# Kernel optimization log

Hardware: AMD Instinct MI355X
Metric: run time of the kernel (lower is better)

Reference implementation:

```python
import jax, jax.numpy as jnp
import numpy as np

N_NODES, N_FEAT, EIG, HID = 20000, 128, 32, 64
N_EDGES = 640000
TEMP = 1.0
NUM_DROP = int(N_NODES * N_FEAT * 0.1)  # num_drop_ratio = 0.1
EPS_LOG = 1e-8


def setup_inputs() -> dict:
    key = jax.random.key(0)
    ks = jax.random.split(key, 9)
    x = jax.random.normal(ks[0], (N_NODES, N_FEAT), dtype=jnp.float32)
    edge_index = jax.random.randint(ks[1], (2, N_EDGES), 0, N_NODES, dtype=jnp.int64)
    edge_weights = jax.random.uniform(ks[2], (N_EDGES,), dtype=jnp.float32)
    x_eigen_distance = jax.random.normal(ks[3], (N_NODES, N_FEAT, EIG), dtype=jnp.float32)
    uni_rand = jax.random.uniform(ks[4], (N_NODES * N_FEAT, 2), dtype=jnp.float32,
                                  minval=1e-6, maxval=1.0 - 1e-6)
    # prob_encoder params: Linear(EIG->HID), ReLU, Linear(HID->2)
    W1 = jax.random.normal(ks[5], (EIG, HID), dtype=jnp.float32) / np.sqrt(EIG)
    b1 = jnp.zeros((HID,), dtype=jnp.float32)
    W2 = jax.random.normal(ks[6], (HID, 2), dtype=jnp.float32) / np.sqrt(HID)
    b2 = jnp.zeros((2,), dtype=jnp.float32)
    return {"x": x, "edge_index": edge_index, "edge_weights": edge_weights,
            "x_eigen_distance": x_eigen_distance, "uni_rand": uni_rand,
            "W1": W1, "b1": b1, "W2": W2, "b2": b2}


def reference(x, edge_index, edge_weights, x_eigen_distance, uni_rand, W1, b1, W2, b2):
    # flatten to [N_NODES*N_FEAT, EIG]
    flat = x_eigen_distance.reshape(-1, x_eigen_distance.shape[-1])
    h = jax.nn.relu(flat @ W1 + b1)          # [M, HID]
    logits = h @ W2 + b2                     # [M, 2]
    logits = jnp.log(jax.nn.softmax(logits, axis=1) + EPS_LOG)
    gumbel = -jnp.log(-jnp.log(uni_rand))    # gumbel noise from uniform
    y = jax.nn.softmax((logits + gumbel) / TEMP, axis=1)
    poss = jnp.clip(1.0 - y[:, 0], 1e-6, 1.0)  # [M]
    neg_vals, idx = jax.lax.top_k(-poss, NUM_DROP)  # smallest NUM_DROP
    vals = -neg_vals
    x_new = x.reshape(-1).at[idx].multiply(vals).reshape(x.shape)
    return x_new, edge_index, edge_weights
```

## Files before the change

kernel.cpp:

```cpp
#include <hip/hip_runtime.h>
#include <hip/hip_bf16.h>

#define N_NODES 20000
#define N_FEAT  128
#define EIG     32
#define HID     64
#define N_EDGES 640000
#define M_ROWS  (N_NODES * N_FEAT)
#define K_DROP  256000
#define NBINS   16384
#define LIST_CAP 4096
#define NTILES  (M_ROWS / 16)
#define NBLK    2560

#define POSS_BYTES ((size_t)M_ROWS * 4)
#define HIST_BYTES (NBINS * 4)
#define META_WORDS 16

typedef __attribute__((ext_vector_type(8))) short short8;
typedef __attribute__((ext_vector_type(4))) float floatx4;

__device__ __forceinline__ short f2bf(float f) {
  unsigned u = __float_as_uint(f);
  unsigned r = u + 0x7fffu + ((u >> 16) & 1u);
  return (short)(r >> 16);
}

__device__ __forceinline__ short2 f2bf2(float x, float y) {
  float2 f; f.x = x; f.y = y;
  __hip_bfloat162 h = __float22bfloat162_rn(f);
  union { __hip_bfloat162 h2; short2 s2; } u;
  u.h2 = h;
  return u.s2;
}

__device__ __forceinline__ int bin_of(float ps) {
  int b = (int)(ps * (float)NBINS);
  if (b > NBINS - 1) b = NBINS - 1;
  if (b < 0) b = 0;
  return b;
}

__global__ __launch_bounds__(256) void poss_kernel(
    const float* __restrict__ eig, const float* __restrict__ uni,
    const float* __restrict__ W1, const float* __restrict__ b1,
    const float* __restrict__ W2, const float* __restrict__ b2,
    float* __restrict__ poss, unsigned* __restrict__ hist)
{
  const int wave = threadIdx.x >> 6;
  const int lane = threadIdx.x & 63;
  const int col  = lane & 15;
  const int quad = lane >> 4;
  const int STR  = NBLK * 4;

  short8 bfrag[4];
  #pragma unroll
  for (int t = 0; t < 4; ++t)
    #pragma unroll
    for (int j = 0; j < 8; ++j)
      bfrag[t][j] = f2bf(W1[(quad * 8 + j) * HID + 16 * t + col]);

  float b1v[4], wd[4];
  #pragma unroll
  for (int t = 0; t < 4; ++t) {
    int n = 16 * t + col;
    b1v[t] = b1[n];
    wd[t] = W2[2 * n + 1] - W2[2 * n + 0];
  }
  const float bd = b2[1] - b2[0];

  const bool epi = (col < 4);
  const int  epirow = quad * 4 + col;

  int tile = blockIdx.x * 4 + wave;
  float4 v0 = {0,0,0,0}, v1 = {0,0,0,0};
  float2 u0 = {0.5f, 0.5f};
  if (tile < NTILES) {
    const float4* pa = (const float4*)(eig + (size_t)(tile * 16 + col) * EIG + quad * 8);
    v0 = pa[0]; v1 = pa[1];
    if (epi) u0 = *(const float2*)(uni + (size_t)(tile * 16 + epirow) * 2);
  }

  for (; tile < NTILES; tile += STR) {
    const int nxt = tile + STR;
    float4 n0 = {0,0,0,0}, n1 = {0,0,0,0};
    float2 nu = {0.5f, 0.5f};
    if (nxt < NTILES) {
      const float4* pn = (const float4*)(eig + (size_t)(nxt * 16 + col) * EIG + quad * 8);
      n0 = pn[0]; n1 = pn[1];
      if (epi) nu = *(const float2*)(uni + (size_t)(nxt * 16 + epirow) * 2);
    }

    const int rowbase = tile * 16;
    union { short8 v; short2 h[4]; } au;
    au.h[0] = f2bf2(v0.x, v0.y);
    au.h[1] = f2bf2(v0.z, v0.w);
    au.h[2] = f2bf2(v1.x, v1.y);
    au.h[3] = f2bf2(v1.z, v1.w);

    floatx4 c[4];
    const floatx4 z = {0.f, 0.f, 0.f, 0.f};
    #pragma unroll
    for (int t = 0; t < 4; ++t)
      c[t] = __builtin_amdgcn_mfma_f32_16x16x32_bf16(au.v, bfrag[t], z, 0, 0, 0);

    float pd[4] = {0, 0, 0, 0};
    #pragma unroll
    for (int t = 0; t < 4; ++t)
      #pragma unroll
      for (int r = 0; r < 4; ++r) {
        float h = fmaxf(c[t][r] + b1v[t], 0.0f);
        pd[r] = fmaf(h, wd[t], pd[r]);
      }

    #pragma unroll
    for (int s = 1; s < 16; s <<= 1)
      #pragma unroll
      for (int r = 0; r < 4; ++r)
        pd[r] += __shfl_xor(pd[r], s, 64);

    if (epi) {
      int r = col;
      float ldiff = ((r == 0) ? pd[0] : (r == 1) ? pd[1] : (r == 2) ? pd[2] : pd[3]) + bd;
      int row = rowbase + epirow;

      float t = __expf(ldiff);
      float e1t = 1e-8f * (1.0f + t);
      float A = t + e1t;
      float B = 1.0f + e1t;
      float Lx = -__logf(u0.x);
      float Ly = -__logf(u0.y);
      float num = A * Lx;
      float ps = __fdividef(num, num + B * Ly);
      ps = fminf(fmaxf(ps, 1e-6f), 1.0f);
      poss[row] = ps;
      atomicAdd(&hist[bin_of(ps)], 1u);
    }

    v0 = n0; v1 = n1; u0 = nu;
  }
}

__global__ void scan_kernel(const unsigned* __restrict__ hist, unsigned* __restrict__ meta)
{
  __shared__ unsigned psum[256];
  __shared__ unsigned chunkbins[64];
  __shared__ unsigned selc, selcum;
  int t = threadIdx.x;
  unsigned s = 0;
  #pragma unroll 4
  for (int i = 0; i < NBINS / 256; ++i) s += hist[t * (NBINS / 256) + i];
  psum[t] = s;
  __syncthreads();
  for (int off = 1; off < 256; off <<= 1) {
    unsigned add = (t >= off) ? psum[t - off] : 0u;
    __syncthreads();
    psum[t] += add;
    __syncthreads();
  }
  unsigned incl = psum[t];
  unsigned excl = incl - s;
  if (excl < K_DROP && K_DROP <= incl) { selc = (unsigned)t; selcum = excl; }
  __syncthreads();
  unsigned c = selc;
  if (t < NBINS / 256) chunkbins[t] = hist[c * (NBINS / 256) + t];
  __syncthreads();
  if (t == 0) {
    unsigned cum = selcum;
    int b = (int)c * (NBINS / 256);
    for (int i = 0; i < NBINS / 256; ++i) {
      unsigned h = chunkbins[i];
      if (cum + h >= K_DROP) { meta[0] = (unsigned)(b + i); meta[1] = cum; break; }
      cum += h;
    }
  }
}

__global__ __launch_bounds__(256) void collect_kernel(
    const float* __restrict__ poss, unsigned* __restrict__ meta,
    unsigned* __restrict__ list,
    const int* __restrict__ ei, const float* __restrict__ ew,
    float* __restrict__ out)
{
  int i = blockIdx.x * 256 + threadIdx.x;
  if (i < M_ROWS / 4) {
    float4 p = ((const float4*)poss)[i];
    int B = (int)meta[0];
    float pp[4] = {p.x, p.y, p.z, p.w};
    #pragma unroll
    for (int j = 0; j < 4; ++j) {
      if (bin_of(pp[j]) == B) {
        unsigned q = atomicAdd(&meta[7], 1u);
        if (q < LIST_CAP) list[q] = (unsigned)(4 * i + j);
      }
    }
  } else {
    int j = (i - M_ROWS / 4) * 4;
    if (j < 2 * N_EDGES) {
      int4 e = *(const int4*)(ei + j);
      *(float4*)(out + M_ROWS + j) =
          make_float4((float)e.x, (float)e.y, (float)e.z, (float)e.w);
    } else {
      int k = j - 2 * N_EDGES;
      *(float4*)(out + M_ROWS + j) = *(const float4*)(ew + k);
    }
  }
}

__global__ void rank_kernel(const float* __restrict__ poss,
                            const unsigned* __restrict__ list,
                            unsigned* __restrict__ meta)
{
  __shared__ unsigned sk[LIST_CAP];
  __shared__ unsigned si[LIST_CAP];
  unsigned n = meta[7];
  if (n > LIST_CAP) n = LIST_CAP;
  unsigned target = K_DROP - meta[1] - 1;
  int t = threadIdx.x;
  for (unsigned i = t; i < n; i += 256) {
    unsigned ix = list[i];
    si[i] = ix;
    sk[i] = __float_as_uint(poss[ix]);
  }
  __syncthreads();
  for (unsigned el = t; el < n; el += 256) {
    unsigned k = sk[el], ix = si[el];
    unsigned r = 0;
    for (unsigned j = 0; j < n; ++j)
      r += (sk[j] < k) || (sk[j] == k && si[j] < ix);
    if (r == target) { meta[2] = k; meta[3] = ix; }
  }
}

__global__ __launch_bounds__(256) void finalize_kernel(
    const float* __restrict__ x, const float* __restrict__ poss,
    const unsigned* __restrict__ meta, float* __restrict__ out)
{
  int i = blockIdx.x * 256 + threadIdx.x;
  if (i >= M_ROWS / 4) return;
  unsigned T = meta[2], cut = meta[3];
  float4 xv = ((const float4*)x)[i];
  float4 pv = ((const float4*)poss)[i];
  float xx[4] = {xv.x, xv.y, xv.z, xv.w};
  float pp[4] = {pv.x, pv.y, pv.z, pv.w};
  float o[4];
  #pragma unroll
  for (int j = 0; j < 4; ++j) {
    unsigned k = __float_as_uint(pp[j]);
    unsigned idx = (unsigned)(4 * i + j);
    bool sel = (k < T) || (k == T && idx <= cut);
    o[j] = sel ? xx[j] * pp[j] : xx[j];
  }
  ((float4*)out)[i] = make_float4(o[0], o[1], o[2], o[3]);
}

extern "C" void kernel_launch(void* const* d_in, const int* in_sizes, int n_in,
                              void* d_out, int out_size, void* d_ws, size_t ws_size,
                              hipStream_t stream)
{
  const float* x   = (const float*)d_in[0];
  const int*   ei  = (const int*)d_in[1];
  const float* ew  = (const float*)d_in[2];
  const float* eig = (const float*)d_in[3];
  const float* uni = (const float*)d_in[4];
  const float* W1  = (const float*)d_in[5];
  const float* b1  = (const float*)d_in[6];
  const float* W2  = (const float*)d_in[7];
  const float* b2  = (const float*)d_in[8];
  float* out = (float*)d_out;

  char* ws = (char*)d_ws;
  float*    poss = (float*)ws;
  unsigned* hist = (unsigned*)(ws + POSS_BYTES);
  unsigned* meta = (unsigned*)(ws + POSS_BYTES + HIST_BYTES);
  unsigned* list = (unsigned*)(ws + POSS_BYTES + HIST_BYTES + META_WORDS * 4);

  hipMemsetAsync(hist, 0, HIST_BYTES + META_WORDS * 4 + LIST_CAP * 4, stream);
  poss_kernel<<<NBLK, 256, 0, stream>>>(eig, uni, W1, b1, W2, b2, poss, hist);
  scan_kernel<<<1, 256, 0, stream>>>(hist, meta);
  collect_kernel<<<2500 + 1875, 256, 0, stream>>>(poss, meta, list, ei, ew, out);
  rank_kernel<<<1, 256, 0, stream>>>(poss, list, meta);
  finalize_kernel<<<2500, 256, 0, stream>>>(x, poss, meta, out);
}
```

Baseline: 532.0 us.

## Fuse collect with finalize and fold edge copy into scan launch

The threshold-bin collection now also writes the output. Elements below the boundary bin are scaled directly, and the single-block rank kernel fixes up only the boundary-bin elements after finding the cut. The edge_index/edge_weights copy moves into extra blocks of the scan launch. This removes one full pass over poss and x and one kernel launch. In exchange, the serial single-block rank step now also does scattered writes.

```diff
diff --git a/kernel.cpp b/kernel.cpp
--- a/kernel.cpp
+++ b/kernel.cpp
@@ -141,8 +141,24 @@
   }
 }
 
-__global__ void scan_kernel(const unsigned* __restrict__ hist, unsigned* __restrict__ meta)
-{
+__global__ __launch_bounds__(256) void scan_edge_kernel(
+    const unsigned* __restrict__ hist, unsigned* __restrict__ meta,
+    const int* __restrict__ ei, const float* __restrict__ ew,
+    float* __restrict__ out)
+{
+  if (blockIdx.x != 0) {
+    int j = (blockIdx.x - 1) * 1024 + threadIdx.x * 4;
+    if (j < 2 * N_EDGES) {
+      int4 e = *(const int4*)(ei + j);
+      *(float4*)(out + M_ROWS + j) =
+          make_float4((float)e.x, (float)e.y, (float)e.z, (float)e.w);
+    } else {
+      int k = j - 2 * N_EDGES;
+      *(float4*)(out + M_ROWS + j) = *(const float4*)(ew + k);
+    }
+    return;
+  }
+
   __shared__ unsigned psum[256];
   __shared__ unsigned chunkbins[64];
   __shared__ unsigned selc, selcum;
@@ -176,43 +192,38 @@
   }
 }
 
-__global__ __launch_bounds__(256) void collect_kernel(
-    const float* __restrict__ poss, unsigned* __restrict__ meta,
-    unsigned* __restrict__ list,
-    const int* __restrict__ ei, const float* __restrict__ ew,
+__global__ __launch_bounds__(256) void collect_fin_kernel(
+    const float* __restrict__ poss, const float* __restrict__ x,
+    unsigned* __restrict__ meta, unsigned* __restrict__ list,
     float* __restrict__ out)
 {
   int i = blockIdx.x * 256 + threadIdx.x;
-  if (i < M_ROWS / 4) {
-    float4 p = ((const float4*)poss)[i];
-    int B = (int)meta[0];
-    float pp[4] = {p.x, p.y, p.z, p.w};
-    #pragma unroll
-    for (int j = 0; j < 4; ++j) {
-      if (bin_of(pp[j]) == B) {
-        unsigned q = atomicAdd(&meta[7], 1u);
-        if (q < LIST_CAP) list[q] = (unsigned)(4 * i + j);
-      }
-    }
-  } else {
-    int j = (i - M_ROWS / 4) * 4;
-    if (j < 2 * N_EDGES) {
-      int4 e = *(const int4*)(ei + j);
-      *(float4*)(out + M_ROWS + j) =
-          make_float4((float)e.x, (float)e.y, (float)e.z, (float)e.w);
-    } else {
-      int k = j - 2 * N_EDGES;
-      *(float4*)(out + M_ROWS + j) = *(const float4*)(ew + k);
-    }
-  }
-}
-
-__global__ void rank_kernel(const float* __restrict__ poss,
-                            const unsigned* __restrict__ list,
-                            unsigned* __restrict__ meta)
+  float4 p = ((const float4*)poss)[i];
+  float4 xv = ((const float4*)x)[i];
+  int B = (int)meta[0];
+  float pp[4] = {p.x, p.y, p.z, p.w};
+  float xx[4] = {xv.x, xv.y, xv.z, xv.w};
+  float o[4];
+  #pragma unroll
+  for (int j = 0; j < 4; ++j) {
+    int b = bin_of(pp[j]);
+    o[j] = (b < B) ? xx[j] * pp[j] : xx[j];
+    if (b == B) {
+      unsigned q = atomicAdd(&meta[7], 1u);
+      if (q < LIST_CAP) list[q] = (unsigned)(4 * i + j);
+    }
+  }
+  ((float4*)out)[i] = make_float4(o[0], o[1], o[2], o[3]);
+}
+
+__global__ __launch_bounds__(256) void rank_fix_kernel(
+    const float* __restrict__ poss, const float* __restrict__ x,
+    const unsigned* __restrict__ list, unsigned* __restrict__ meta,
+    float* __restrict__ out)
 {
   __shared__ unsigned sk[LIST_CAP];
   __shared__ unsigned si[LIST_CAP];
+  __shared__ unsigned sT, sCut;
   unsigned n = meta[7];
   if (n > LIST_CAP) n = LIST_CAP;
   unsigned target = K_DROP - meta[1] - 1;
@@ -228,30 +239,15 @@
     unsigned r = 0;
     for (unsigned j = 0; j < n; ++j)
       r += (sk[j] < k) || (sk[j] == k && si[j] < ix);
-    if (r == target) { meta[2] = k; meta[3] = ix; }
-  }
-}
-
-__global__ __launch_bounds__(256) void finalize_kernel(
-    const float* __restrict__ x, const float* __restrict__ poss,
-    const unsigned* __restrict__ meta, float* __restrict__ out)
-{
-  int i = blockIdx.x * 256 + threadIdx.x;
-  if (i >= M_ROWS / 4) return;
-  unsigned T = meta[2], cut = meta[3];
-  float4 xv = ((const float4*)x)[i];
-  float4 pv = ((const float4*)poss)[i];
-  float xx[4] = {xv.x, xv.y, xv.z, xv.w};
-  float pp[4] = {pv.x, pv.y, pv.z, pv.w};
-  float o[4];
-  #pragma unroll
-  for (int j = 0; j < 4; ++j) {
-    unsigned k = __float_as_uint(pp[j]);
-    unsigned idx = (unsigned)(4 * i + j);
-    bool sel = (k < T) || (k == T && idx <= cut);
-    o[j] = sel ? xx[j] * pp[j] : xx[j];
-  }
-  ((float4*)out)[i] = make_float4(o[0], o[1], o[2], o[3]);
+    if (r == target) { sT = k; sCut = ix; meta[2] = k; meta[3] = ix; }
+  }
+  __syncthreads();
+  unsigned T = sT, cut = sCut;
+  for (unsigned i = t; i < n; i += 256) {
+    unsigned ix = si[i], k = sk[i];
+    bool sel = (k < T) || (k == T && ix <= cut);
+    if (sel) out[ix] = x[ix] * __uint_as_float(k);
+  }
 }
 
 extern "C" void kernel_launch(void* const* d_in, const int* in_sizes, int n_in,
@@ -277,8 +273,7 @@
 
   hipMemsetAsync(hist, 0, HIST_BYTES + META_WORDS * 4 + LIST_CAP * 4, stream);
   poss_kernel<<<NBLK, 256, 0, stream>>>(eig, uni, W1, b1, W2, b2, poss, hist);
-  scan_kernel<<<1, 256, 0, stream>>>(hist, meta);
-  collect_kernel<<<2500 + 1875, 256, 0, stream>>>(poss, meta, list, ei, ew, out);
-  rank_kernel<<<1, 256, 0, stream>>>(poss, list, meta);
-  finalize_kernel<<<2500, 256, 0, stream>>>(x, poss, meta, out);
-}
+  scan_edge_kernel<<<1876, 256, 0, stream>>>(hist, meta, ei, ew, out);
+  collect_fin_kernel<<<M_ROWS / 1024, 256, 0, stream>>>(poss, x, meta, list, out);
+  rank_fix_kernel<<<1, 256, 0, stream>>>(poss, x, list, meta, out);
+}
```

Result: no change. 531.7 us (-0.0%).
